# Performance work log

Hardware: AMD Instinct MI355X
Metric: run time of the kernel (lower is better)

The kernel has to match this reference:

```python
import jax, jax.numpy as jnp
from jax import lax
import numpy as np

B, C_IN, IMG = 32, 4, 224
FH = FW = IMG // 8  # 28: three stride-2 maxpools
NA = 4
SCORE_T, IOU_T, MAXP = 0.7, 0.3, 10
EPS = 1e-5


def conv2d(x, w, b, pad):
    y = lax.conv_general_dilated(x, w, (1, 1), [(pad, pad), (pad, pad)],
                                 dimension_numbers=('NCHW', 'OIHW', 'NCHW'))
    return y + b[None, :, None, None]


def bn_eval(x, g, b):
    # eval-mode BN with running_mean=0, running_var=1 (fresh model), eps=1e-5
    return x * (g / jnp.sqrt(1.0 + EPS))[None, :, None, None] + b[None, :, None, None]


def maxpool2(x):
    return lax.reduce_window(x, -jnp.inf, lax.max, (1, 1, 2, 2), (1, 1, 2, 2), 'VALID')


def make_anchors():
    ys = (jnp.arange(FH) + 0.5) / FH
    xs = (jnp.arange(FW) + 0.5) / FW
    cy, cx = jnp.meshgrid(ys, xs, indexing='ij')
    cxy = jnp.stack([cx, cy], -1)  # [H,W,2], matches loop order y,x then anchor
    sizes = jnp.array([[16., 16.], [32., 32.], [64., 64.], [128., 128.]], jnp.float32) / 224.0
    a = jnp.concatenate([jnp.broadcast_to(cxy[:, :, None, :], (FH, FW, NA, 2)),
                         jnp.broadcast_to(sizes[None, None], (FH, FW, NA, 2))], -1)
    return a.reshape(-1, 4)  # [H*W*NA, 4] = [3136, 4]


def decode_boxes(anchors, offsets):
    centers = anchors[..., :2] + offsets[..., :2] * 0.1
    sizes = anchors[..., 2:] * jnp.exp(offsets[..., 2:] * 0.2)
    boxes = jnp.concatenate([centers - sizes / 2, centers + sizes / 2], -1)
    return jnp.clip(boxes, 0.0, 1.0)


def nms_single(boxes, scores):
    # greedy NMS, fixed MAXP iterations (== max_proposals_per_image cap)
    N = scores.shape[0]
    s0 = jnp.where(scores > SCORE_T, scores, -jnp.inf)  # score-threshold filter
    areas = (boxes[:, 2] - boxes[:, 0]) * (boxes[:, 3] - boxes[:, 1])
    idx_all = jnp.arange(N)

    def body(s, _):
        i = jnp.argmax(s)
        ok = s[i] > -jnp.inf
        bi = boxes[i]
        xx1 = jnp.maximum(bi[0], boxes[:, 0]); yy1 = jnp.maximum(bi[1], boxes[:, 1])
        xx2 = jnp.minimum(bi[2], boxes[:, 2]); yy2 = jnp.minimum(bi[3], boxes[:, 3])
        inter = jnp.clip(xx2 - xx1, 0.0) * jnp.clip(yy2 - yy1, 0.0)
        iou = inter / (areas[i] + areas - inter)
        sup = (iou > IOU_T) | (idx_all == i)
        s_next = jnp.where(ok & sup, -jnp.inf, s)
        return s_next, (jnp.where(ok, i, 0), ok)

    _, (idxs, oks) = lax.scan(body, s0, None, length=MAXP)
    return idxs, oks  # [MAXP] int32, [MAXP] bool


def _forward(x, r1w, r1b, g1, b1, r2w, r2b, g2, b2, r3w, r3b, g3, b3, rpw, rpb,
             clsw, clsb, regw, regb, c1w, c1b, cg1, cb1, c2w, c2b, cg2, cb2,
             fc1w, fc1b, fc2w, fc2b, fc3w, fc3b, fc4w, fc4b):
    Bsz = x.shape[0]
    # --- Stage 1: lightweight RPN ---
    h = maxpool2(jax.nn.relu(bn_eval(conv2d(x, r1w, r1b, 1), g1, b1)))
    h = maxpool2(jax.nn.relu(bn_eval(conv2d(h, r2w, r2b, 1), g2, b2)))
    h = maxpool2(jax.nn.relu(bn_eval(conv2d(h, r3w, r3b, 1), g3, b3)))
    h = jax.nn.relu(conv2d(h, rpw, rpb, 1))
    cls = conv2d(h, clsw, clsb, 0).transpose(0, 2, 3, 1).reshape(Bsz, -1, 2)
    reg = conv2d(h, regw, regb, 0).transpose(0, 2, 3, 1).reshape(Bsz, -1, 4)
    anchors = make_anchors()
    probs = jax.nn.softmax(cls, -1)[..., 1]        # [B,N] objectness
    boxes = decode_boxes(anchors[None], reg)       # [B,N,4]
    # --- proposal selection: score threshold + greedy NMS + top-10 cap ---
    idxs, oks = jax.vmap(nms_single)(boxes, probs)  # [B,10]
    okf = oks.astype(boxes.dtype)
    kept_boxes = jax.vmap(lambda b, i: b[i])(boxes, idxs) * okf[..., None]
    kept_scores = jax.vmap(lambda s, i: s[i])(probs, idxs) * okf
    has_prop = (probs > SCORE_T).any(-1)           # [B]
    # --- Stage 2: CLM classifier (applied to the full image, as in original) ---
    f = jax.nn.relu(bn_eval(conv2d(x, c1w, c1b, 1), cg1, cb1))
    f = jax.nn.relu(bn_eval(conv2d(f, c2w, c2b, 1), cg2, cb2))
    # AdaptiveAvgPool2d((7,7)) on 224x224 -> mean over 32x32 blocks
    f = f.reshape(Bsz, 128, 7, 32, 7, 32).mean(axis=(3, 5)).reshape(Bsz, -1)
    f = jax.nn.relu(f @ fc1w + fc1b)
    f = jax.nn.relu(f @ fc2w + fc2b)
    f = jax.nn.relu(f @ fc3w + fc3b)
    logits = f @ fc4w + fc4b
    bg = jnp.array([1.0, 0.0], logits.dtype)
    final = jnp.where(has_prop[:, None], logits, bg[None])
    return final, kept_boxes, kept_scores, oks


def setup_inputs() -> dict:
    key = jax.random.key(0)
    ks = iter(jax.random.split(key, 64))

    def conv_w(o, i, k):
        return jax.random.normal(next(ks), (o, i, k, k), jnp.float32) * float(np.sqrt(2.0 / (i * k * k)))

    def lin_w(i, o):
        return jax.random.normal(next(ks), (i, o), jnp.float32) * float(1.0 / np.sqrt(i))

    return {
        'x': jax.random.normal(next(ks), (B, C_IN, IMG, IMG), jnp.float32),
        'r1w': conv_w(32, 4, 3), 'r1b': jnp.zeros(32), 'g1': jnp.ones(32), 'b1': jnp.zeros(32),
        'r2w': conv_w(64, 32, 3), 'r2b': jnp.zeros(64), 'g2': jnp.ones(64), 'b2': jnp.zeros(64),
        'r3w': conv_w(128, 64, 3), 'r3b': jnp.zeros(128), 'g3': jnp.ones(128), 'b3': jnp.zeros(128),
        'rpw': conv_w(256, 128, 3), 'rpb': jnp.zeros(256),
        'clsw': conv_w(8, 256, 1), 'clsb': jnp.zeros(8),
        'regw': conv_w(16, 256, 1), 'regb': jnp.zeros(16),
        'c1w': conv_w(64, 4, 3), 'c1b': jnp.zeros(64), 'cg1': jnp.ones(64), 'cb1': jnp.zeros(64),
        'c2w': conv_w(128, 64, 3), 'c2b': jnp.zeros(128), 'cg2': jnp.ones(128), 'cb2': jnp.zeros(128),
        'fc1w': lin_w(6272, 512), 'fc1b': jnp.zeros(512),
        'fc2w': lin_w(512, 256), 'fc2b': jnp.zeros(256),
        'fc3w': lin_w(256, 128), 'fc3b': jnp.zeros(128),
        'fc4w': lin_w(128, 2), 'fc4b': jnp.zeros(2),
    }


def reference(x, r1w, r1b, g1, b1, r2w, r2b, g2, b2, r3w, r3b, g3, b3, rpw, rpb,
              clsw, clsb, regw, regb, c1w, c1b, cg1, cb1, c2w, c2b, cg2, cb2,
              fc1w, fc1b, fc2w, fc2b, fc3w, fc3b, fc4w, fc4b):
    return _forward(x, r1w, r1b, g1, b1, r2w, r2b, g2, b2, r3w, r3b, g3, b3, rpw, rpb,
                    clsw, clsb, regw, regb, c1w, c1b, cg1, cb1, c2w, c2b, cg2, cb2,
                    fc1w, fc1b, fc2w, fc2b, fc3w, fc3b, fc4w, fc4b)
```

## Files before the change

kernel.cpp:

```cpp
#include <hip/hip_runtime.h>
#include <math.h>

constexpr int NANCH = 3136;
constexpr float SCORE_T = 0.7f;
constexpr float IOU_T = 0.3f;
constexpr int MAXP = 10;

typedef unsigned short u16;
typedef __attribute__((ext_vector_type(8))) short short8x;
typedef __attribute__((ext_vector_type(4))) float f32x4;

__device__ inline u16 f2bf(float f) {
  unsigned u = __builtin_bit_cast(unsigned, f);
  u += 0x7fffu + ((u >> 16) & 1u);
  return (u16)(u >> 16);
}
__device__ inline float bf2f(u16 h) {
  unsigned u = ((unsigned)h) << 16;
  return __builtin_bit_cast(float, u);
}

template<int CIN, int CK, int OCB, bool BN, int MODE>
__global__ __launch_bounds__(256) void conv_k(
    const float* __restrict__ in, const float* __restrict__ wgt,
    const float* __restrict__ bias, const float* __restrict__ gamma,
    const float* __restrict__ beta, float* __restrict__ out,
    u16* __restrict__ o2hi, u16* __restrict__ o2lo,
    int H, int W, int COUT) {
  const int tid = threadIdx.x;
  const int tx = tid & 15, ty = tid >> 4;
  const int ng = COUT / OCB;
  const int b  = blockIdx.z / ng;
  const int oc0 = (blockIdx.z % ng) * OCB;
  __shared__ float s_in[CK][34][34];
  __shared__ float s_w[CK][3][3][OCB];

  float acc[OCB][2][2];
#pragma unroll
  for (int o = 0; o < OCB; o++) {
    acc[o][0][0] = 0.f; acc[o][0][1] = 0.f; acc[o][1][0] = 0.f; acc[o][1][1] = 0.f;
  }
  const int y0 = blockIdx.y * 32 - 1, x0 = blockIdx.x * 32 - 1;

  for (int ck0 = 0; ck0 < CIN; ck0 += CK) {
    for (int t = tid; t < CK * 34 * 34; t += 256) {
      const int ck = t / 1156; const int r = t % 1156;
      const int iy = r / 34, ix = r % 34;
      const int gy = y0 + iy, gx = x0 + ix;
      float v = 0.f;
      if ((unsigned)gy < (unsigned)H && (unsigned)gx < (unsigned)W)
        v = in[(((size_t)b * CIN + ck0 + ck) * H + gy) * W + gx];
      s_in[ck][iy][ix] = v;
    }
    for (int t = tid; t < CK * 9 * OCB; t += 256) {
      const int oc = t % OCB; int r = t / OCB;
      const int kx = r % 3; r /= 3; const int ky = r % 3; const int ck = r / 3;
      s_w[ck][ky][kx][oc] = wgt[(((size_t)(oc0 + oc) * CIN + (ck0 + ck)) * 3 + ky) * 3 + kx];
    }
    __syncthreads();

#pragma unroll 2
    for (int ck = 0; ck < CK; ck++) {
#pragma unroll
      for (int ky = 0; ky < 3; ky++) {
#pragma unroll
        for (int kx = 0; kx < 3; kx++) {
          float w8[OCB];
#pragma unroll
          for (int o = 0; o < OCB; o++) w8[o] = s_w[ck][ky][kx][o];
          float xv[2][2];
#pragma unroll
          for (int dy = 0; dy < 2; dy++)
#pragma unroll
            for (int dx = 0; dx < 2; dx++)
              xv[dy][dx] = s_in[ck][2 * ty + dy + ky][2 * tx + dx + kx];
#pragma unroll
          for (int o = 0; o < OCB; o++)
#pragma unroll
            for (int dy = 0; dy < 2; dy++)
#pragma unroll
              for (int dx = 0; dx < 2; dx++)
                acc[o][dy][dx] = fmaf(w8[o], xv[dy][dx], acc[o][dy][dx]);
        }
      }
    }
    __syncthreads();
  }

  const float rsq = 1.f / sqrtf(1.f + 1e-5f);

  if (MODE == 3) {
    float bi8[OCB], sc8[OCB], sh8[OCB];
#pragma unroll
    for (int o = 0; o < OCB; o++) {
      bi8[o] = bias[oc0 + o]; sc8[o] = gamma[oc0 + o] * rsq; sh8[o] = beta[oc0 + o];
    }
#pragma unroll
    for (int dy = 0; dy < 2; dy++)
#pragma unroll
      for (int dx = 0; dx < 2; dx++) {
        const int oy = blockIdx.y * 32 + 2 * ty + dy;
        const int ox = blockIdx.x * 32 + 2 * tx + dx;
        u16 u[8];
#pragma unroll
        for (int o = 0; o < OCB; o++)
          u[o] = f2bf(fmaxf((acc[o][dy][dx] + bi8[o]) * sc8[o] + sh8[o], 0.f));
        *(uint4*)&o2hi[(((size_t)b * 224 + oy) * 224 + ox) * 64 + oc0] = *(uint4*)u;
      }
    return;
  }

  if (MODE == 5) {
    const int PH = H >> 1, PW = W >> 1;
    const int py = blockIdx.y * 16 + ty, px = blockIdx.x * 16 + tx;
    u16 uh[8], ul[8];
#pragma unroll
    for (int o = 0; o < OCB; o++) {
      const int oc = oc0 + o;
      const float bi = bias[oc], scl = gamma[oc] * rsq, shf = beta[oc];
      float m = (acc[o][0][0] + bi) * scl + shf;
      m = fmaxf(m, (acc[o][0][1] + bi) * scl + shf);
      m = fmaxf(m, (acc[o][1][0] + bi) * scl + shf);
      m = fmaxf(m, (acc[o][1][1] + bi) * scl + shf);
      m = fmaxf(m, 0.f);
      uh[o] = f2bf(m); ul[o] = f2bf(m - bf2f(uh[o]));
    }
    const size_t base = (((size_t)b * PH + py) * PW + px) * 32 + oc0;
    *(uint4*)&o2hi[base] = *(uint4*)uh;
    *(uint4*)&o2lo[base] = *(uint4*)ul;
    return;
  }

#pragma unroll
  for (int o = 0; o < OCB; o++) {
    const int oc = oc0 + o;
    const float bi = bias[oc];
    float scl = 1.f, shf = 0.f;
    if (BN) { scl = gamma[oc] * rsq; shf = beta[oc]; }

    if (MODE == 0) {
#pragma unroll
      for (int dy = 0; dy < 2; dy++)
#pragma unroll
        for (int dx = 0; dx < 2; dx++) {
          const int oy = blockIdx.y * 32 + 2 * ty + dy;
          const int ox = blockIdx.x * 32 + 2 * tx + dx;
          if (oy < H && ox < W) {
            const float e = (acc[o][dy][dx] + bi) * scl + shf;
            out[(((size_t)b * COUT + oc) * H + oy) * W + ox] = fmaxf(e, 0.f);
          }
        }
    } else if (MODE == 1) {
      const int PH = H >> 1, PW = W >> 1;
      const int py = blockIdx.y * 16 + ty, px = blockIdx.x * 16 + tx;
      if (py < PH && px < PW) {
        float m = (acc[o][0][0] + bi) * scl + shf;
        m = fmaxf(m, (acc[o][0][1] + bi) * scl + shf);
        m = fmaxf(m, (acc[o][1][0] + bi) * scl + shf);
        m = fmaxf(m, (acc[o][1][1] + bi) * scl + shf);
        out[(((size_t)b * COUT + oc) * PH + py) * PW + px] = fmaxf(m, 0.f);
      }
    }
  }
}

__global__ __launch_bounds__(256) void wsplit_k(const float* __restrict__ w,
                                                u16* __restrict__ hi, u16* __restrict__ lo,
                                                int COUT, int CIN) {
  const int n = 9 * COUT * CIN;
  const int i = blockIdx.x * 256 + threadIdx.x;
  if (i >= n) return;
  const int cin = i % CIN; int r = i / CIN;
  const int cout = r % COUT; const int tap = r / COUT;
  const float v = w[((size_t)cout * CIN + cin) * 9 + tap];
  const u16 h = f2bf(v);
  hi[i] = h; lo[i] = f2bf(v - bf2f(h));
}

__global__ __launch_bounds__(256) void w2b_k(const float* __restrict__ w,
                                             u16* __restrict__ wb) {
  const int i = blockIdx.x * 256 + threadIdx.x;
  if (i >= 73728) return;
  const int cin = i & 63; const int r = i >> 6;
  const int cout = r & 127; const int tap = r >> 7;
  wb[i] = f2bf(w[(((size_t)cout * 64 + cin) * 3 + tap / 3) * 3 + tap % 3]);
}

template<int CINCH, bool POOL, bool BN>
__global__ __launch_bounds__(256) void sconv_k(
    const u16* __restrict__ ahi, const u16* __restrict__ alo,
    const u16* __restrict__ whi, const u16* __restrict__ wlo,
    const float* __restrict__ bias, const float* __restrict__ gamma,
    const float* __restrict__ beta,
    u16* __restrict__ ohi, u16* __restrict__ olo, float* __restrict__ of32,
    int H, int W, int COUT, int cog) {
  __shared__ u16 s_in[6 * 34 * 72];
  __shared__ u16 s_w[64 * 72];
  const int tid = threadIdx.x, lane = tid & 63, wave = tid >> 6;
  const int wm = wave >> 1, wn = wave & 1, lr = lane & 15, lg = lane >> 4;
  const int img = blockIdx.z / cog, co0 = (blockIdx.z % cog) * 64;
  const int x0 = blockIdx.x * 32, band = blockIdx.y;
  const int CIN = CINCH * 32;

  f32x4 acc[4][2];
#pragma unroll
  for (int mi = 0; mi < 4; ++mi) { acc[mi][0] = (f32x4)(0.f); acc[mi][1] = (f32x4)(0.f); }

  for (int cc2 = 0; cc2 < CINCH; ++cc2) {
    for (int idx = tid; idx < 1632; idx += 256) {
      const int r = idx / 272, rem = idx % 272;
      const int c = rem >> 3, q = rem & 7, pl = q >> 2, qq = q & 3;
      const int gy = band * 4 - 1 + r, gx = x0 - 1 + c;
      uint4 v = make_uint4(0, 0, 0, 0);
      if ((unsigned)gy < (unsigned)H && (unsigned)gx < (unsigned)W) {
        const u16* src = pl ? alo : ahi;
        v = *(const uint4*)(src + ((size_t)(img * H + gy) * W + gx) * CIN + cc2 * 32 + qq * 8);
      }
      *(uint4*)(&s_in[(r * 34 + c) * 72 + pl * 32 + qq * 8]) = v;
    }
    for (int tap = 0; tap < 9; ++tap) {
      const int ky = tap / 3, kx = tap % 3;
      for (int idx = tid; idx < 512; idx += 256) {
        const int cout = idx >> 3, q = idx & 7, pl = q >> 2, qq = q & 3;
        const u16* src = pl ? wlo : whi;
        uint4 v = *(const uint4*)(src + ((size_t)tap * COUT + co0 + cout) * CIN + cc2 * 32 + qq * 8);
        *(uint4*)(&s_w[cout * 72 + pl * 32 + qq * 8]) = v;
      }
      __syncthreads();
      short8x ah[4], al[4], bh[2], bl[2];
#pragma unroll
      for (int mi = 0; mi < 4; ++mi) {
        const int base = ((2 * wm + (mi >> 1) + ky) * 34 + (mi & 1) * 16 + lr + kx) * 72;
        ah[mi] = *(const short8x*)(&s_in[base + lg * 8]);
        al[mi] = *(const short8x*)(&s_in[base + 32 + lg * 8]);
      }
#pragma unroll
      for (int ni = 0; ni < 2; ++ni) {
        const int wb2 = (wn * 32 + ni * 16 + lr) * 72;
        bh[ni] = *(const short8x*)(&s_w[wb2 + lg * 8]);
        bl[ni] = *(const short8x*)(&s_w[wb2 + 32 + lg * 8]);
      }
#pragma unroll
      for (int mi = 0; mi < 4; ++mi)
#pragma unroll
        for (int ni = 0; ni < 2; ++ni) {
          acc[mi][ni] = __builtin_amdgcn_mfma_f32_16x16x32_bf16(al[mi], bh[ni], acc[mi][ni], 0, 0, 0);
          acc[mi][ni] = __builtin_amdgcn_mfma_f32_16x16x32_bf16(ah[mi], bl[ni], acc[mi][ni], 0, 0, 0);
          acc[mi][ni] = __builtin_amdgcn_mfma_f32_16x16x32_bf16(ah[mi], bh[ni], acc[mi][ni], 0, 0, 0);
        }
      __syncthreads();
    }
  }

  const float rsq = 1.f / sqrtf(1.f + 1e-5f);
#pragma unroll
  for (int ni = 0; ni < 2; ++ni) {
    const int cout = co0 + wn * 32 + ni * 16 + lr;
    const float bi = bias[cout];
    const float scl = BN ? gamma[cout] * rsq : 1.f;
    const float shf = BN ? beta[cout] : 0.f;
    if (POOL) {
      const int OH = H >> 1, OW = W >> 1;
      const int py = band * 2 + wm;
#pragma unroll
      for (int ch = 0; ch < 2; ++ch)
#pragma unroll
        for (int jp = 0; jp < 2; ++jp) {
          float m = (acc[ch][ni][2 * jp] + bi) * scl + shf;
          m = fmaxf(m, (acc[ch][ni][2 * jp + 1] + bi) * scl + shf);
          m = fmaxf(m, (acc[ch + 2][ni][2 * jp] + bi) * scl + shf);
          m = fmaxf(m, (acc[ch + 2][ni][2 * jp + 1] + bi) * scl + shf);
          m = fmaxf(m, 0.f);
          const int px = (x0 >> 1) + ch * 8 + lg * 2 + jp;
          if (px < OW) {
            const size_t o = ((size_t)(img * OH + py) * OW + px) * COUT + cout;
            const u16 h = f2bf(m);
            ohi[o] = h; olo[o] = f2bf(m - bf2f(h));
          }
        }
    } else {
#pragma unroll
      for (int mi = 0; mi < 4; ++mi) {
        const int row = band * 4 + 2 * wm + (mi >> 1);
#pragma unroll
        for (int j = 0; j < 4; ++j) {
          const int px = x0 + (mi & 1) * 16 + lg * 4 + j;
          if (px < W)
            of32[((size_t)(img * H + row) * W + px) * COUT + cout] =
                fmaxf(acc[mi][ni][j] + bi, 0.f);
        }
      }
    }
  }
}

__global__ __launch_bounds__(256) void c2band_k(
    const u16* __restrict__ act, const u16* __restrict__ wb,
    const float* __restrict__ bias, const float* __restrict__ gamma,
    const float* __restrict__ beta, float* __restrict__ pooled, int gimg0) {
  __shared__ u16 s_in[6 * 34 * 72];
  __shared__ u16 s_w[2 * 128 * 40];
  __shared__ float s_pool[128];

  const int tid = threadIdx.x;
  const int lane = tid & 63, wave = tid >> 6;
  const int wm = wave >> 1, wn = wave & 1;
  const int lr = lane & 15, lg = lane >> 4;
  const int img = blockIdx.z >> 3, band = blockIdx.z & 7;
  const int x0 = blockIdx.x * 32, y0 = blockIdx.y * 32;
  const float rsq = 1.f / sqrtf(1.f + 1e-5f);

  if (tid < 128) s_pool[tid] = 0.f;

  for (int idx = tid; idx < 1632; idx += 256) {
    const int r = idx / 272, rem = idx % 272;
    const int c = rem >> 3, q = rem & 7;
    const int gy = y0 + band * 4 - 1 + r, gx = x0 - 1 + c;
    uint4 v = make_uint4(0, 0, 0, 0);
    if ((unsigned)gy < 224u && (unsigned)gx < 224u)
      v = *(const uint4*)(act + (((size_t)img * 224 + gy) * 224 + gx) * 64 + q * 8);
    *(uint4*)(&s_in[(r * 34 + c) * 72 + q * 8]) = v;
  }

  f32x4 acc[4][4];
#pragma unroll
  for (int mi = 0; mi < 4; ++mi)
#pragma unroll
    for (int ni = 0; ni < 4; ++ni) acc[mi][ni] = (f32x4)(0.f);

  for (int tap = 0; tap < 9; ++tap) {
    const int ky = tap / 3, kx = tap % 3;
    for (int idx = tid; idx < 1024; idx += 256) {
      const int cout = idx >> 3, q = idx & 7;
      uint4 v = *(const uint4*)(wb + ((size_t)tap * 128 + cout) * 64 + q * 8);
      *(uint4*)(&s_w[(q >> 2) * 5120 + cout * 40 + (q & 3) * 8]) = v;
    }
    __syncthreads();
#pragma unroll
    for (int h = 0; h < 2; ++h) {
      short8x a[4], bf[4];
#pragma unroll
      for (int mi = 0; mi < 4; ++mi) {
        const int rl = wm * 2 + (mi >> 1) + ky;
        const int cc = (mi & 1) * 16 + lr + kx;
        a[mi] = *(const short8x*)(&s_in[(rl * 34 + cc) * 72 + h * 32 + lg * 8]);
      }
#pragma unroll
      for (int ni = 0; ni < 4; ++ni) {
        const int co = wn * 64 + ni * 16 + lr;
        bf[ni] = *(const short8x*)(&s_w[h * 5120 + co * 40 + lg * 8]);
      }
#pragma unroll
      for (int mi = 0; mi < 4; ++mi)
#pragma unroll
        for (int ni = 0; ni < 4; ++ni)
          acc[mi][ni] = __builtin_amdgcn_mfma_f32_16x16x32_bf16(a[mi], bf[ni], acc[mi][ni], 0, 0, 0);
    }
    __syncthreads();
  }
#pragma unroll
  for (int ni = 0; ni < 4; ++ni) {
    const int co = wn * 64 + ni * 16 + lr;
    const float bi = bias[co], scl = gamma[co] * rsq, shf = beta[co];
    float s = 0.f;
#pragma unroll
    for (int mi = 0; mi < 4; ++mi)
#pragma unroll
      for (int j = 0; j < 4; ++j)
        s += fmaxf((acc[mi][ni][j] + bi) * scl + shf, 0.f);
    atomicAdd(&s_pool[co], s);
  }
  __syncthreads();
  if (tid < 128)
    atomicAdd(&pooled[(size_t)(gimg0 + img) * 6272 + tid * 49 + blockIdx.y * 7 + blockIdx.x],
              s_pool[tid] * (1.f / 1024.f));
}

__global__ __launch_bounds__(256) void rpn_head_k(
    const float* __restrict__ feat,
    const float* __restrict__ clsw, const float* __restrict__ clsb,
    const float* __restrict__ regw, const float* __restrict__ regb,
    float* __restrict__ probs, float* __restrict__ boxes) {
  const int gid = blockIdx.x * 256 + threadIdx.x;
  if (gid >= 32 * NANCH) return;
  const int a = gid & 3;
  int r = gid >> 2;
  const int x = r % 28; r /= 28;
  const int y = r % 28;
  const int b = r / 28;

  const float* f = feat + ((size_t)b * 784 + y * 28 + x) * 256;
  float c0 = clsb[2 * a], c1 = clsb[2 * a + 1];
  float r0 = regb[4 * a], r1 = regb[4 * a + 1], r2 = regb[4 * a + 2], r3 = regb[4 * a + 3];
#pragma unroll 4
  for (int c = 0; c < 256; c++) {
    const float fv = f[c];
    c0 = fmaf(fv, clsw[(2 * a) * 256 + c], c0);
    c1 = fmaf(fv, clsw[(2 * a + 1) * 256 + c], c1);
    r0 = fmaf(fv, regw[(4 * a) * 256 + c], r0);
    r1 = fmaf(fv, regw[(4 * a + 1) * 256 + c], r1);
    r2 = fmaf(fv, regw[(4 * a + 2) * 256 + c], r2);
    r3 = fmaf(fv, regw[(4 * a + 3) * 256 + c], r3);
  }
  const float p = 1.f / (1.f + expf(c0 - c1));

  const float cx = (x + 0.5f) * (1.f / 28.f);
  const float cy = (y + 0.5f) * (1.f / 28.f);
  const float sz = (float)(16 << a) * (1.f / 224.f);
  const float ncx = cx + r0 * 0.1f, ncy = cy + r1 * 0.1f;
  const float nw = sz * expf(r2 * 0.2f), nh = sz * expf(r3 * 0.2f);
  const float x1 = fminf(fmaxf(ncx - nw * 0.5f, 0.f), 1.f);
  const float y1 = fminf(fmaxf(ncy - nh * 0.5f, 0.f), 1.f);
  const float x2 = fminf(fmaxf(ncx + nw * 0.5f, 0.f), 1.f);
  const float y2 = fminf(fmaxf(ncy + nh * 0.5f, 0.f), 1.f);

  probs[gid] = p;
  ((float4*)boxes)[gid] = make_float4(x1, y1, x2, y2);
}

__global__ __launch_bounds__(256) void nms_k(
    const float* __restrict__ probs, const float* __restrict__ boxes,
    float* __restrict__ dout, int* __restrict__ hasflag) {
  const int b = blockIdx.x;
  const int t = threadIdx.x;
  __shared__ float sc[NANCH];
  __shared__ float ar[NANCH];
  __shared__ float4 bx[NANCH];
  __shared__ float rv[256];
  __shared__ int   ri[256];
  __shared__ int s_any, s_sel[MAXP], s_ok[MAXP];

  if (t == 0) s_any = 0;
  __syncthreads();

  int anyl = 0;
  for (int i = t; i < NANCH; i += 256) {
    const float p = probs[(size_t)b * NANCH + i];
    const float4 bb = ((const float4*)boxes)[(size_t)b * NANCH + i];
    bx[i] = bb;
    ar[i] = (bb.z - bb.x) * (bb.w - bb.y);
    sc[i] = (p > SCORE_T) ? p : -INFINITY;
    if (p > SCORE_T) anyl = 1;
  }
  if (anyl) atomicOr(&s_any, 1);
  __syncthreads();

  for (int it = 0; it < MAXP; ++it) {
    float bv = -INFINITY; int bi = 0x7fffffff;
    for (int i = t; i < NANCH; i += 256) {
      const float v = sc[i];
      if (v > bv || (v == bv && i < bi)) { bv = v; bi = i; }
    }
    rv[t] = bv; ri[t] = bi;
    __syncthreads();
    for (int st = 128; st > 0; st >>= 1) {
      if (t < st) {
        const float ov = rv[t + st]; const int oi = ri[t + st];
        if (ov > rv[t] || (ov == rv[t] && oi < ri[t])) { rv[t] = ov; ri[t] = oi; }
      }
      __syncthreads();
    }
    if (t == 0) { s_sel[it] = ri[0]; s_ok[it] = (rv[0] > -INFINITY) ? 1 : 0; }
    __syncthreads();
    const int sel = s_sel[it];
    const int ok  = s_ok[it];
    if (ok) {
      const float4 bs = bx[sel]; const float as = ar[sel];
      for (int i = t; i < NANCH; i += 256) {
        const float xx1 = fmaxf(bs.x, bx[i].x), yy1 = fmaxf(bs.y, bx[i].y);
        const float xx2 = fminf(bs.z, bx[i].z), yy2 = fminf(bs.w, bx[i].w);
        const float inter = fmaxf(xx2 - xx1, 0.f) * fmaxf(yy2 - yy1, 0.f);
        const float iou = inter / (as + ar[i] - inter);
        if (iou > IOU_T || i == sel) sc[i] = -INFINITY;
      }
    }
    __syncthreads();
  }

  if (t < MAXP) {
    const int sel = s_ok[t] ? s_sel[t] : 0;
    const float okf = s_ok[t] ? 1.f : 0.f;
    const float4 bb = bx[sel];
    float* kb = dout + 64;
    float* ks = dout + 64 + 32 * MAXP * 4;
    float* ko = dout + 64 + 32 * MAXP * 5;
    const size_t base = ((size_t)b * MAXP + t) * 4;
    kb[base + 0] = bb.x * okf; kb[base + 1] = bb.y * okf;
    kb[base + 2] = bb.z * okf; kb[base + 3] = bb.w * okf;
    ks[b * MAXP + t] = probs[(size_t)b * NANCH + sel] * okf;
    ko[b * MAXP + t] = okf;
  }
  if (t == 0) hasflag[b] = s_any;
}

__global__ __launch_bounds__(64) void fcsplit_k(
    const float* __restrict__ x, const float* __restrict__ w,
    float* __restrict__ part, int K, int N, int kchunk) {
  extern __shared__ float sx[];
  const int o = blockIdx.x * 64 + threadIdx.x;
  const int k0 = blockIdx.y * kchunk;
  for (int i = threadIdx.x; i < 32 * kchunk; i += 64) {
    const int bb = i / kchunk, kk = i % kchunk;
    sx[i] = x[(size_t)bb * K + k0 + kk];
  }
  __syncthreads();
  float acc[32];
#pragma unroll
  for (int bb = 0; bb < 32; bb++) acc[bb] = 0.f;
#pragma unroll 8
  for (int kk = 0; kk < kchunk; kk++) {
    const float wv = w[(size_t)(k0 + kk) * N + o];
#pragma unroll
    for (int bb = 0; bb < 32; bb++) acc[bb] = fmaf(sx[bb * kchunk + kk], wv, acc[bb]);
  }
  float* p = part + (size_t)blockIdx.y * 32 * N + o;
#pragma unroll
  for (int bb = 0; bb < 32; bb++) p[(size_t)bb * N] = acc[bb];
}

__global__ __launch_bounds__(256) void fcreduce_k(
    const float* __restrict__ part, const float* __restrict__ bias,
    float* __restrict__ y, int N, int KT, int dorelu) {
  const int i = blockIdx.x * 256 + threadIdx.x;
  if (i >= 32 * N) return;
  const int o = i % N;
  float s = bias[o];
  for (int kt = 0; kt < KT; kt++) s += part[(size_t)kt * 32 * N + i];
  y[i] = dorelu ? fmaxf(s, 0.f) : s;
}

__global__ __launch_bounds__(64) void final_k(
    const float* __restrict__ f3, const float* __restrict__ w,
    const float* __restrict__ bi, const int* __restrict__ hasflag,
    float* __restrict__ dout) {
  const int t = threadIdx.x;
  if (t >= 64) return;
  const int b = t >> 1, j = t & 1;
  float acc = bi[j];
#pragma unroll 4
  for (int k = 0; k < 128; k++) acc = fmaf(f3[b * 128 + k], w[k * 2 + j], acc);
  dout[b * 2 + j] = hasflag[b] ? acc : (j == 0 ? 1.f : 0.f);
}

extern "C" void kernel_launch(void* const* d_in, const int* in_sizes, int n_in,
                              void* d_out, int out_size, void* d_ws, size_t ws_size,
                              hipStream_t stream) {
  const float* x    = (const float*)d_in[0];
  const float* r1w  = (const float*)d_in[1];  const float* r1b = (const float*)d_in[2];
  const float* g1   = (const float*)d_in[3];  const float* b1  = (const float*)d_in[4];
  const float* r2w  = (const float*)d_in[5];  const float* r2b = (const float*)d_in[6];
  const float* g2   = (const float*)d_in[7];  const float* b2  = (const float*)d_in[8];
  const float* r3w  = (const float*)d_in[9];  const float* r3b = (const float*)d_in[10];
  const float* g3   = (const float*)d_in[11]; const float* b3  = (const float*)d_in[12];
  const float* rpw  = (const float*)d_in[13]; const float* rpb = (const float*)d_in[14];
  const float* clsw = (const float*)d_in[15]; const float* clsb = (const float*)d_in[16];
  const float* regw = (const float*)d_in[17]; const float* regb = (const float*)d_in[18];
  const float* c1w  = (const float*)d_in[19]; const float* c1b = (const float*)d_in[20];
  const float* cg1  = (const float*)d_in[21]; const float* cb1 = (const float*)d_in[22];
  const float* c2w  = (const float*)d_in[23]; const float* c2b = (const float*)d_in[24];
  const float* cg2  = (const float*)d_in[25]; const float* cb2 = (const float*)d_in[26];
  const float* fc1w = (const float*)d_in[27]; const float* fc1b = (const float*)d_in[28];
  const float* fc2w = (const float*)d_in[29]; const float* fc2b = (const float*)d_in[30];
  const float* fc3w = (const float*)d_in[31]; const float* fc3b = (const float*)d_in[32];
  const float* fc4w = (const float*)d_in[33]; const float* fc4b = (const float*)d_in[34];
  float* dout = (float*)d_out;
  float* Wp = (float*)d_ws;

  const size_t o_h1   = 0;
  const size_t o_h2   = 12845056;
  const size_t o_h3   = o_h2 + 6422528;
  const size_t o_prob = o_h3 + 3211264;
  const size_t o_box  = o_prob + 100352;
  const size_t o_flag = o_box + 401408;
  const size_t o_pool = o_flag + 32;
  const size_t o_f1   = o_pool + 200704;
  const size_t o_f2   = o_f1 + 16384;
  const size_t o_f3   = o_f2 + 8192;
  const size_t o_w2b  = o_f3 + 4096;
  const size_t o_w2s  = o_w2b + 36864;
  const size_t o_w3s  = o_w2s + 18432;
  const size_t o_wps  = o_w3s + 73728;

  u16* h1hi = (u16*)(Wp + o_h1); u16* h1lo = h1hi + 12845056;
  u16* h2hi = (u16*)(Wp + o_h2); u16* h2lo = h2hi + 6422528;
  u16* h3hi = (u16*)(Wp + o_h3); u16* h3lo = h3hi + 3211264;
  float* probs = Wp + o_prob; float* boxes = Wp + o_box;
  int* hasflag = (int*)(Wp + o_flag);
  float* pooled = Wp + o_pool;
  float* f1 = Wp + o_f1; float* f2 = Wp + o_f2; float* f3 = Wp + o_f3;
  u16* w2b  = (u16*)(Wp + o_w2b);
  u16* w2hi = (u16*)(Wp + o_w2s); u16* w2lo = w2hi + 18432;
  u16* w3hi = (u16*)(Wp + o_w3s); u16* w3lo = w3hi + 73728;
  u16* wphi = (u16*)(Wp + o_wps); u16* wplo = wphi + 294912;
  float* h4f32 = Wp + o_h1;
  u16*   c1buf = (u16*)(Wp + o_h1);
  float* fcpart = Wp + o_h1;

  wsplit_k<<<(9 * 64 * 32 + 255) / 256, 256, 0, stream>>>(r2w, w2hi, w2lo, 64, 32);
  wsplit_k<<<(9 * 128 * 64 + 255) / 256, 256, 0, stream>>>(r3w, w3hi, w3lo, 128, 64);
  wsplit_k<<<(9 * 256 * 128 + 255) / 256, 256, 0, stream>>>(rpw, wphi, wplo, 256, 128);
  w2b_k<<<288, 256, 0, stream>>>(c2w, w2b);

  conv_k<4, 4, 8, true, 5><<<dim3(7, 7, 32 * 4), 256, 0, stream>>>(
      x, r1w, r1b, g1, b1, Wp, h1hi, h1lo, 224, 224, 32);
  sconv_k<1, true, true><<<dim3(4, 28, 32), 256, 0, stream>>>(
      h1hi, h1lo, w2hi, w2lo, r2b, g2, b2, h2hi, h2lo, nullptr, 112, 112, 64, 1);
  sconv_k<2, true, true><<<dim3(2, 14, 64), 256, 0, stream>>>(
      h2hi, h2lo, w3hi, w3lo, r3b, g3, b3, h3hi, h3lo, nullptr, 56, 56, 128, 2);
  sconv_k<4, false, false><<<dim3(1, 7, 128), 256, 0, stream>>>(
      h3hi, h3lo, wphi, wplo, rpb, rpb, rpb, nullptr, nullptr, h4f32, 28, 28, 256, 4);

  rpn_head_k<<<(32 * NANCH + 255) / 256, 256, 0, stream>>>(h4f32, clsw, clsb, regw, regb, probs, boxes);
  nms_k<<<32, 256, 0, stream>>>(probs, boxes, dout, hasflag);

  hipMemsetAsync(pooled, 0, 32 * 6272 * sizeof(float), stream);
  constexpr int CHUNK = 8;
  for (int c0 = 0; c0 < 32; c0 += CHUNK) {
    conv_k<4, 4, 8, true, 3><<<dim3(7, 7, CHUNK * 8), 256, 0, stream>>>(
        x + (size_t)c0 * 4 * 224 * 224, c1w, c1b, cg1, cb1, Wp, c1buf, nullptr, 224, 224, 64);
    c2band_k<<<dim3(7, 7, CHUNK * 8), 256, 0, stream>>>(
        c1buf, w2b, c2b, cg2, cb2, pooled, c0);
  }

  fcsplit_k<<<dim3(8, 64), 64, 32 * 98 * 4, stream>>>(pooled, fc1w, fcpart, 6272, 512, 98);
  fcreduce_k<<<64, 256, 0, stream>>>(fcpart, fc1b, f1, 512, 64, 1);
  fcsplit_k<<<dim3(4, 16), 64, 32 * 32 * 4, stream>>>(f1, fc2w, fcpart, 512, 256, 32);
  fcreduce_k<<<32, 256, 0, stream>>>(fcpart, fc2b, f2, 256, 16, 1);
  fcsplit_k<<<dim3(2, 8), 64, 32 * 32 * 4, stream>>>(f2, fc3w, fcpart, 256, 128, 32);
  fcreduce_k<<<16, 256, 0, stream>>>(fcpart, fc3b, f3, 128, 8, 1);
  final_k<<<1, 64, 0, stream>>>(f3, fc4w, fc4b, hasflag, dout);
}
```

Measured before the change: 1.340 ms.

## Replace scalar first-layer convolutions with bf16 MFMA im2col kernels

```diff
diff --git a/kernel.cpp b/kernel.cpp
--- a/kernel.cpp
+++ b/kernel.cpp
@@ -20,146 +20,146 @@
   return __builtin_bit_cast(float, u);
 }
 
-template<int CIN, int CK, int OCB, bool BN, int MODE>
-__global__ __launch_bounds__(256) void conv_k(
-    const float* __restrict__ in, const float* __restrict__ wgt,
+__global__ __launch_bounds__(256) void w1prep_k(const float* __restrict__ w,
+                                                u16* __restrict__ hi, u16* __restrict__ lo,
+                                                int COUT) {
+  const int i = blockIdx.x * 256 + threadIdx.x;
+  if (i >= COUT * 64) return;
+  const int k = i & 63, co = i >> 6;
+  float v = 0.f;
+  if (k < 36) { const int tap = k >> 2, cin = k & 3; v = w[co * 36 + cin * 9 + tap]; }
+  const u16 h = f2bf(v);
+  hi[i] = h;
+  lo[i] = f2bf(v - bf2f(h));
+}
+
+template<int MODE>
+__global__ __launch_bounds__(256) void c1mfma_k(
+    const float* __restrict__ x,
+    const u16* __restrict__ wfh, const u16* __restrict__ wfl,
     const float* __restrict__ bias, const float* __restrict__ gamma,
-    const float* __restrict__ beta, float* __restrict__ out,
-    u16* __restrict__ o2hi, u16* __restrict__ o2lo,
-    int H, int W, int COUT) {
-  const int tid = threadIdx.x;
-  const int tx = tid & 15, ty = tid >> 4;
-  const int ng = COUT / OCB;
-  const int b  = blockIdx.z / ng;
-  const int oc0 = (blockIdx.z % ng) * OCB;
-  __shared__ float s_in[CK][34][34];
-  __shared__ float s_w[CK][3][3][OCB];
-
-  float acc[OCB][2][2];
-#pragma unroll
-  for (int o = 0; o < OCB; o++) {
-    acc[o][0][0] = 0.f; acc[o][0][1] = 0.f; acc[o][1][0] = 0.f; acc[o][1][1] = 0.f;
-  }
-  const int y0 = blockIdx.y * 32 - 1, x0 = blockIdx.x * 32 - 1;
-
-  for (int ck0 = 0; ck0 < CIN; ck0 += CK) {
-    for (int t = tid; t < CK * 34 * 34; t += 256) {
-      const int ck = t / 1156; const int r = t % 1156;
-      const int iy = r / 34, ix = r % 34;
-      const int gy = y0 + iy, gx = x0 + ix;
-      float v = 0.f;
-      if ((unsigned)gy < (unsigned)H && (unsigned)gx < (unsigned)W)
-        v = in[(((size_t)b * CIN + ck0 + ck) * H + gy) * W + gx];
-      s_in[ck][iy][ix] = v;
-    }
-    for (int t = tid; t < CK * 9 * OCB; t += 256) {
-      const int oc = t % OCB; int r = t / OCB;
-      const int kx = r % 3; r /= 3; const int ky = r % 3; const int ck = r / 3;
-      s_w[ck][ky][kx][oc] = wgt[(((size_t)(oc0 + oc) * CIN + (ck0 + ck)) * 3 + ky) * 3 + kx];
+    const float* __restrict__ beta,
+    u16* __restrict__ outhi, u16* __restrict__ outlo) {
+  constexpr int COUT = MODE ? 32 : 64;
+  constexpr int NF   = MODE ? 2 : 4;
+  constexpr int PS   = MODE ? 136 : 72;
+  __shared__ u16 s_patch[64 * PS];
+  __shared__ u16 s_wh[COUT * 72];
+  __shared__ u16 s_wl[MODE ? COUT * 72 : 8];
+  __shared__ float s_raw[4 * 6 * 18];
+  __shared__ float s_pool[MODE ? 4 * 16 * 17 : 1];
+  __shared__ u16 s_out[MODE ? 8 : 64 * 72];
+
+  const int tid = threadIdx.x, lane = tid & 63, w = tid >> 6;
+  const int lr = lane & 15, lg = lane >> 4;
+  const int img = blockIdx.z;
+  const int x0 = blockIdx.x * 16, y0 = blockIdx.y * 4;
+
+  for (int i = tid; i < 64 * 7; i += 256) {
+    const int p = i / 7, q = i % 7;
+    *(uint2*)&s_patch[p * PS + 36 + q * 4] = make_uint2(0, 0);
+    if (MODE) *(uint2*)&s_patch[p * PS + 100 + q * 4] = make_uint2(0, 0);
+  }
+  for (int i = tid; i < 432; i += 256) {
+    const int cin = i / 108, r = i % 108;
+    const int ry = r / 18, rx = r % 18;
+    const int gy = y0 - 1 + ry, gx = x0 - 1 + rx;
+    float v = 0.f;
+    if ((unsigned)gy < 224u && (unsigned)gx < 224u)
+      v = x[(((size_t)img * 4 + cin) * 224 + gy) * 224 + gx];
+    s_raw[i] = v;
+  }
+  for (int i = tid; i < COUT * 8; i += 256) {
+    const int co = i >> 3, q = i & 7;
+    *(uint4*)&s_wh[co * 72 + q * 8] = *(const uint4*)&wfh[co * 64 + q * 8];
+    if (MODE) *(uint4*)&s_wl[co * 72 + q * 8] = *(const uint4*)&wfl[co * 64 + q * 8];
+  }
+  __syncthreads();
+
+  for (int i = tid; i < 576; i += 256) {
+    const int p = i / 9, tap = i % 9;
+    const int ty = p >> 4, tx = p & 15;
+    const int ky = tap / 3, kx = tap % 3;
+    u16 h4[4], l4[4];
+#pragma unroll
+    for (int cin = 0; cin < 4; cin++) {
+      const float v = s_raw[cin * 108 + (ty + ky) * 18 + (tx + kx)];
+      h4[cin] = f2bf(v);
+      if (MODE) l4[cin] = f2bf(v - bf2f(h4[cin]));
+    }
+    *(uint2*)&s_patch[p * PS + tap * 4] = *(uint2*)h4;
+    if (MODE) *(uint2*)&s_patch[p * PS + 64 + tap * 4] = *(uint2*)l4;
+  }
+  __syncthreads();
+
+  int pA;
+  if (MODE) pA = ((w >> 1) * 2 + (lr >> 3)) * 16 + (w & 1) * 8 + (lr & 7);
+  else      pA = w * 16 + lr;
+
+  f32x4 acc[NF];
+#pragma unroll
+  for (int nf = 0; nf < NF; nf++) acc[nf] = (f32x4)(0.f);
+
+#pragma unroll
+  for (int ks = 0; ks < 2; ks++) {
+    const short8x ah = *(const short8x*)&s_patch[pA * PS + ks * 32 + lg * 8];
+    short8x al;
+    if (MODE) al = *(const short8x*)&s_patch[pA * PS + 64 + ks * 32 + lg * 8];
+#pragma unroll
+    for (int nf = 0; nf < NF; nf++) {
+      const short8x bh = *(const short8x*)&s_wh[(nf * 16 + lr) * 72 + ks * 32 + lg * 8];
+      if (MODE) {
+        const short8x bl = *(const short8x*)&s_wl[(nf * 16 + lr) * 72 + ks * 32 + lg * 8];
+        acc[nf] = __builtin_amdgcn_mfma_f32_16x16x32_bf16(al, bh, acc[nf], 0, 0, 0);
+        acc[nf] = __builtin_amdgcn_mfma_f32_16x16x32_bf16(ah, bl, acc[nf], 0, 0, 0);
+      }
+      acc[nf] = __builtin_amdgcn_mfma_f32_16x16x32_bf16(ah, bh, acc[nf], 0, 0, 0);
+    }
+  }
+
+  const float rsq = 1.f / sqrtf(1.f + 1e-5f);
+
+  if (MODE == 0) {
+#pragma unroll
+    for (int nf = 0; nf < 4; nf++) {
+      const int co = nf * 16 + lr;
+      const float bi = bias[co], scl = gamma[co] * rsq, shf = beta[co];
+#pragma unroll
+      for (int j = 0; j < 4; j++) {
+        const float e = fmaxf((acc[nf][j] + bi) * scl + shf, 0.f);
+        s_out[(w * 16 + lg * 4 + j) * 72 + co] = f2bf(e);
+      }
     }
     __syncthreads();
-
-#pragma unroll 2
-    for (int ck = 0; ck < CK; ck++) {
-#pragma unroll
-      for (int ky = 0; ky < 3; ky++) {
-#pragma unroll
-        for (int kx = 0; kx < 3; kx++) {
-          float w8[OCB];
-#pragma unroll
-          for (int o = 0; o < OCB; o++) w8[o] = s_w[ck][ky][kx][o];
-          float xv[2][2];
-#pragma unroll
-          for (int dy = 0; dy < 2; dy++)
-#pragma unroll
-            for (int dx = 0; dx < 2; dx++)
-              xv[dy][dx] = s_in[ck][2 * ty + dy + ky][2 * tx + dx + kx];
-#pragma unroll
-          for (int o = 0; o < OCB; o++)
-#pragma unroll
-            for (int dy = 0; dy < 2; dy++)
-#pragma unroll
-              for (int dx = 0; dx < 2; dx++)
-                acc[o][dy][dx] = fmaf(w8[o], xv[dy][dx], acc[o][dy][dx]);
-        }
-      }
-    }
-    __syncthreads();
-  }
-
-  const float rsq = 1.f / sqrtf(1.f + 1e-5f);
-
-  if (MODE == 3) {
-    float bi8[OCB], sc8[OCB], sh8[OCB];
-#pragma unroll
-    for (int o = 0; o < OCB; o++) {
-      bi8[o] = bias[oc0 + o]; sc8[o] = gamma[oc0 + o] * rsq; sh8[o] = beta[oc0 + o];
-    }
-#pragma unroll
-    for (int dy = 0; dy < 2; dy++)
-#pragma unroll
-      for (int dx = 0; dx < 2; dx++) {
-        const int oy = blockIdx.y * 32 + 2 * ty + dy;
-        const int ox = blockIdx.x * 32 + 2 * tx + dx;
-        u16 u[8];
-#pragma unroll
-        for (int o = 0; o < OCB; o++)
-          u[o] = f2bf(fmaxf((acc[o][dy][dx] + bi8[o]) * sc8[o] + sh8[o], 0.f));
-        *(uint4*)&o2hi[(((size_t)b * 224 + oy) * 224 + ox) * 64 + oc0] = *(uint4*)u;
-      }
-    return;
-  }
-
-  if (MODE == 5) {
-    const int PH = H >> 1, PW = W >> 1;
-    const int py = blockIdx.y * 16 + ty, px = blockIdx.x * 16 + tx;
-    u16 uh[8], ul[8];
-#pragma unroll
-    for (int o = 0; o < OCB; o++) {
-      const int oc = oc0 + o;
-      const float bi = bias[oc], scl = gamma[oc] * rsq, shf = beta[oc];
-      float m = (acc[o][0][0] + bi) * scl + shf;
-      m = fmaxf(m, (acc[o][0][1] + bi) * scl + shf);
-      m = fmaxf(m, (acc[o][1][0] + bi) * scl + shf);
-      m = fmaxf(m, (acc[o][1][1] + bi) * scl + shf);
-      m = fmaxf(m, 0.f);
-      uh[o] = f2bf(m); ul[o] = f2bf(m - bf2f(uh[o]));
-    }
-    const size_t base = (((size_t)b * PH + py) * PW + px) * 32 + oc0;
-    *(uint4*)&o2hi[base] = *(uint4*)uh;
-    *(uint4*)&o2lo[base] = *(uint4*)ul;
-    return;
-  }
-
-#pragma unroll
-  for (int o = 0; o < OCB; o++) {
-    const int oc = oc0 + o;
-    const float bi = bias[oc];
-    float scl = 1.f, shf = 0.f;
-    if (BN) { scl = gamma[oc] * rsq; shf = beta[oc]; }
-
-    if (MODE == 0) {
-#pragma unroll
-      for (int dy = 0; dy < 2; dy++)
-#pragma unroll
-        for (int dx = 0; dx < 2; dx++) {
-          const int oy = blockIdx.y * 32 + 2 * ty + dy;
-          const int ox = blockIdx.x * 32 + 2 * tx + dx;
-          if (oy < H && ox < W) {
-            const float e = (acc[o][dy][dx] + bi) * scl + shf;
-            out[(((size_t)b * COUT + oc) * H + oy) * W + ox] = fmaxf(e, 0.f);
-          }
-        }
-    } else if (MODE == 1) {
-      const int PH = H >> 1, PW = W >> 1;
-      const int py = blockIdx.y * 16 + ty, px = blockIdx.x * 16 + tx;
-      if (py < PH && px < PW) {
-        float m = (acc[o][0][0] + bi) * scl + shf;
-        m = fmaxf(m, (acc[o][0][1] + bi) * scl + shf);
-        m = fmaxf(m, (acc[o][1][0] + bi) * scl + shf);
-        m = fmaxf(m, (acc[o][1][1] + bi) * scl + shf);
-        out[(((size_t)b * COUT + oc) * PH + py) * PW + px] = fmaxf(m, 0.f);
-      }
+    for (int i = tid; i < 512; i += 256) {
+      const int p = i >> 3, q = i & 7;
+      const int oy = y0 + (p >> 4), ox = x0 + (p & 15);
+      *(uint4*)&outhi[(((size_t)img * 224 + oy) * 224 + ox) * 64 + q * 8] =
+          *(uint4*)&s_out[p * 72 + q * 8];
+    }
+  } else {
+#pragma unroll
+    for (int nf = 0; nf < 2; nf++) {
+      const int co = nf * 16 + lr;
+      const float bi = bias[co], scl = gamma[co] * rsq, shf = beta[co];
+#pragma unroll
+      for (int j = 0; j < 4; j++) {
+        const int m = lg * 4 + j;
+        s_pool[w * 272 + m * 17 + lr] = (acc[nf][j] + bi) * scl + shf;
+      }
+      __syncthreads();
+      {
+        const int pc = lane >> 4, n = lane & 15;
+        const float* sp = &s_pool[w * 272];
+        float m0 = fmaxf(sp[(pc * 2) * 17 + n], sp[(pc * 2 + 1) * 17 + n]);
+        float m1 = fmaxf(sp[(pc * 2 + 8) * 17 + n], sp[(pc * 2 + 9) * 17 + n]);
+        const float mm = fmaxf(fmaxf(m0, m1), 0.f);
+        const int py = (y0 >> 1) + (w >> 1), px = (x0 >> 1) + (w & 1) * 4 + pc;
+        const size_t o = (((size_t)img * 112 + py) * 112 + px) * 32 + nf * 16 + n;
+        const u16 h = f2bf(mm);
+        outhi[o] = h; outlo[o] = f2bf(mm - bf2f(h));
+      }
+      __syncthreads();
     }
   }
 }
@@ -580,6 +580,8 @@
   const size_t o_w2s  = o_w2b + 36864;
   const size_t o_w3s  = o_w2s + 18432;
   const size_t o_wps  = o_w3s + 73728;
+  const size_t o_w1r  = o_wps + 294912;
+  const size_t o_w1c  = o_w1r + 2048;
 
   u16* h1hi = (u16*)(Wp + o_h1); u16* h1lo = h1hi + 12845056;
   u16* h2hi = (u16*)(Wp + o_h2); u16* h2lo = h2hi + 6422528;
@@ -592,6 +594,8 @@
   u16* w2hi = (u16*)(Wp + o_w2s); u16* w2lo = w2hi + 18432;
   u16* w3hi = (u16*)(Wp + o_w3s); u16* w3lo = w3hi + 73728;
   u16* wphi = (u16*)(Wp + o_wps); u16* wplo = wphi + 294912;
+  u16* w1rhi = (u16*)(Wp + o_w1r); u16* w1rlo = w1rhi + 2048;
+  u16* w1chi = (u16*)(Wp + o_w1c); u16* w1clo = w1chi + 4096;
   float* h4f32 = Wp + o_h1;
   u16*   c1buf = (u16*)(Wp + o_h1);
   float* fcpart = Wp + o_h1;
@@ -600,9 +604,11 @@
   wsplit_k<<<(9 * 128 * 64 + 255) / 256, 256, 0, stream>>>(r3w, w3hi, w3lo, 128, 64);
   wsplit_k<<<(9 * 256 * 128 + 255) / 256, 256, 0, stream>>>(rpw, wphi, wplo, 256, 128);
   w2b_k<<<288, 256, 0, stream>>>(c2w, w2b);
-
-  conv_k<4, 4, 8, true, 5><<<dim3(7, 7, 32 * 4), 256, 0, stream>>>(
-      x, r1w, r1b, g1, b1, Wp, h1hi, h1lo, 224, 224, 32);
+  w1prep_k<<<8, 256, 0, stream>>>(r1w, w1rhi, w1rlo, 32);
+  w1prep_k<<<16, 256, 0, stream>>>(c1w, w1chi, w1clo, 64);
+
+  c1mfma_k<1><<<dim3(14, 56, 32), 256, 0, stream>>>(
+      x, w1rhi, w1rlo, r1b, g1, b1, h1hi, h1lo);
   sconv_k<1, true, true><<<dim3(4, 28, 32), 256, 0, stream>>>(
       h1hi, h1lo, w2hi, w2lo, r2b, g2, b2, h2hi, h2lo, nullptr, 112, 112, 64, 1);
   sconv_k<2, true, true><<<dim3(2, 14, 64), 256, 0, stream>>>(
@@ -616,8 +622,8 @@
   hipMemsetAsync(pooled, 0, 32 * 6272 * sizeof(float), stream);
   constexpr int CHUNK = 8;
   for (int c0 = 0; c0 < 32; c0 += CHUNK) {
-    conv_k<4, 4, 8, true, 3><<<dim3(7, 7, CHUNK * 8), 256, 0, stream>>>(
-        x + (size_t)c0 * 4 * 224 * 224, c1w, c1b, cg1, cb1, Wp, c1buf, nullptr, 224, 224, 64);
+    c1mfma_k<0><<<dim3(14, 56, CHUNK), 256, 0, stream>>>(
+        x + (size_t)c0 * 4 * 224 * 224, w1chi, w1clo, c1b, cg1, cb1, c1buf, nullptr);
     c2band_k<<<dim3(7, 7, CHUNK * 8), 256, 0, stream>>>(
         c1buf, w2b, c2b, cg2, cb2, pooled, c0);
   }
```

Result: faster. 1.162 ms (-13.3%).
